# Optimization experiments

Hardware: AMD Instinct MI355X
Metric: run time of the kernel (lower is better)

## Reference

```python
import jax, jax.numpy as jnp
import numpy as np

ENC_HID = 512
DEC_HID = 1024
ATTN_DIM = 1024
ATTN_IN = ENC_HID * 2 + DEC_HID  # 2048
B, S = 32, 1024


def setup_inputs() -> dict:
    key = jax.random.key(0)
    k1, k2, k3, k4, k5 = jax.random.split(key, 5)
    decoder_hidden = jax.random.normal(k1, (B, DEC_HID), dtype=jnp.float32)
    encoder_outputs = jax.random.normal(k2, (B, S, 2 * ENC_HID), dtype=jnp.float32)
    # nn.Linear(attn_in, attn_dim): weight [attn_dim, attn_in], bias [attn_dim]
    lim = 1.0 / np.sqrt(ATTN_IN)
    W = jax.random.uniform(k3, (ATTN_IN, ATTN_DIM), jnp.float32, -lim, lim)
    b = jax.random.uniform(k4, (ATTN_DIM,), jnp.float32, -lim, lim)
    v = jax.random.uniform(k5, (ATTN_DIM,), jnp.float32, 0.0, 1.0)
    return {"decoder_hidden": decoder_hidden, "encoder_outputs": encoder_outputs,
            "W": W, "b": b, "v": v}


def reference(decoder_hidden, encoder_outputs, W, b, v):
    # Avoid materializing the repeat+concat: split the Linear weight into the
    # decoder-hidden block and the encoder-outputs block. Same math as
    # tanh(Linear(cat([dec_rep, enc], -1))).
    W_dec = W[:DEC_HID]          # [dec_hid, attn_dim]
    W_enc = W[DEC_HID:]          # [2*enc_hid, attn_dim]
    dec_proj = decoder_hidden @ W_dec + b                     # [B, A]
    enc_proj = jnp.einsum('bse,ea->bsa', encoder_outputs, W_enc)  # [B, S, A]
    energy = jnp.tanh(enc_proj + dec_proj[:, None, :])        # [B, S, A]
    attention = jnp.einsum('bsa,a->bs', energy, v)            # [B, S]
    return jax.nn.softmax(attention, axis=1)
```

## Files before the change

### kernel.cpp

```cpp
#include <hip/hip_runtime.h>
#include <stdint.h>

#define ENC2 1024
#define DECH 1024
#define ADIM 1024
#define BB   32
#define SS   1024

typedef _Float16 half_t;
typedef __attribute__((ext_vector_type(8))) _Float16 half8;
typedef __attribute__((ext_vector_type(4))) float    f32x4;

__device__ __forceinline__ void dma16(const half_t* g, half_t* l) {
    __builtin_amdgcn_global_load_lds((const __attribute__((address_space(1))) void*)g,
                                     (__attribute__((address_space(3))) void*)l,
                                     16, 0, 0);
}

__global__ __launch_bounds__(256) void k_wt(const float* __restrict__ W,
                                            half_t* __restrict__ Wt2) {
    __shared__ float tile[32][257];
    const int nb = blockIdx.x >> 5;
    const int ks = blockIdx.x & 31;
    const int t = threadIdx.x;
    #pragma unroll
    for (int i = 0; i < 32; i++) {
        int idx = t + i * 256;
        int kr = idx >> 8, n = idx & 255;
        tile[kr][n] = W[(size_t)(DECH + ks * 32 + kr) * ADIM + nb * 256 + n];
    }
    __syncthreads();
    half_t* reg = Wt2 + ((size_t)(nb * 32 + ks) << 13);
    #pragma unroll
    for (int i = 0; i < 4; i++) {
        int cid = t + i * 256;
        int r = cid >> 2, pos = cid & 3;
        int c = pos ^ ((r >> 1) & 3);
        half8 h;
        #pragma unroll
        for (int e = 0; e < 8; e++) h[e] = (half_t)tile[c * 8 + e][r];
        *(half8*)(reg + r * 32 + pos * 8) = h;
    }
}

__global__ __launch_bounds__(256) void k_dp1(const float* __restrict__ dh,
                                             const float* __restrict__ W,
                                             float* __restrict__ part) {
    __shared__ float red[4][BB][64];
    const int t = threadIdx.x;
    const int ct = blockIdx.x & 15;
    const int kc = blockIdx.x >> 4;
    const int col = ct * 64 + (t & 63);
    const int w = t >> 6;
    const int k0 = kc * 128 + w * 32;
    float wreg[32];
    #pragma unroll
    for (int kk = 0; kk < 32; kk++)
        wreg[kk] = W[(size_t)(k0 + kk) * ADIM + col];
    float s[BB];
    #pragma unroll
    for (int b = 0; b < BB; b++) s[b] = 0.f;
    #pragma unroll
    for (int kk = 0; kk < 32; kk++) {
        #pragma unroll
        for (int b = 0; b < BB; b++)
            s[b] += dh[b * DECH + k0 + kk] * wreg[kk];
    }
    #pragma unroll
    for (int b = 0; b < BB; b++) red[w][b][t & 63] = s[b];
    __syncthreads();
    if (t < 64) {
        for (int b = 0; b < BB; b++)
            part[((size_t)kc * BB + b) * ADIM + ct * 64 + t] =
                red[0][b][t] + red[1][b][t] + red[2][b][t] + red[3][b][t];
    }
}

__global__ __launch_bounds__(256) void k_dp2(const float* __restrict__ part,
                                             const float* __restrict__ bias,
                                             float* __restrict__ decp) {
    const int i = blockIdx.x * 256 + threadIdx.x;
    float s = bias[i & (ADIM - 1)];
    #pragma unroll
    for (int kc = 0; kc < 8; kc++)
        s += part[(size_t)kc * BB * ADIM + i];
    decp[i] = s;
}

#define BM 128
#define BN 256
#define BK 32
#define LDA 40

__global__ __launch_bounds__(512, 4) void k_main(const float* __restrict__ enc,
                                                 const half_t* __restrict__ Wt2,
                                                 const float* __restrict__ decp,
                                                 const float* __restrict__ v,
                                                 float* __restrict__ scores_part) {
    __shared__ half_t lsA[2][BM][LDA];
    __shared__ half_t lsB[2][BN * BK];

    const int bid = blockIdx.x;
    const int mi = (bid >> 5) * 8 + (bid & 7);
    const int nb = (bid >> 3) & 3;
    const int m0 = mi * BM;
    const int t = threadIdx.x;
    const int w = t >> 6, L = t & 63;
    const int wm = w & 1, wn = w >> 1;
    const int lane15 = L & 15, quad = L >> 4;

    const int arow = t & 127;
    const int akc  = (t >> 7) * 8;
    const float* Aptr = enc + (size_t)(m0 + arow) * ENC2 + akc;

    const half_t* Bbase = Wt2 + ((size_t)(nb * 32) << 13);

    f32x4 acc[4][4];
    #pragma unroll
    for (int i = 0; i < 4; i++)
        #pragma unroll
        for (int j = 0; j < 4; j++) acc[i][j] = (f32x4)0.f;

    float4 ra0, ra1;
    auto loadA = [&](int ks) {
        const float* p = Aptr + ks * BK;
        ra0 = *(const float4*)p;
        ra1 = *(const float4*)(p + 4);
    };
    auto writeA = [&](int pb) {
        half8 ha;
        ha[0] = (half_t)ra0.x; ha[1] = (half_t)ra0.y;
        ha[2] = (half_t)ra0.z; ha[3] = (half_t)ra0.w;
        ha[4] = (half_t)ra1.x; ha[5] = (half_t)ra1.y;
        ha[6] = (half_t)ra1.z; ha[7] = (half_t)ra1.w;
        *(half8*)&lsA[pb][arow][akc] = ha;
    };
    auto dmaB = [&](int ks, int pb) {
        #pragma unroll
        for (int jj = 0; jj < 2; jj++) {
            int j = 2 * w + jj;
            dma16(Bbase + ((size_t)ks << 13) + j * 512 + L * 8,
                  &lsB[pb][j * 512]);
        }
    };

    dmaB(0, 0);
    loadA(0);
    writeA(0);
    loadA(1);
    __syncthreads();

    for (int ks = 0; ks < ENC2 / BK; ks++) {
        const int cur = ks & 1;
        if (ks < ENC2 / BK - 1) {
            dmaB(ks + 1, cur ^ 1);
            writeA(cur ^ 1);
            if (ks < ENC2 / BK - 2) loadA(ks + 2);
        }
        half8 af[4], bf[4];
        #pragma unroll
        for (int sm = 0; sm < 4; sm++)
            af[sm] = *(const half8*)&lsA[cur][wm * 64 + sm * 16 + lane15][quad * 8];
        #pragma unroll
        for (int sn = 0; sn < 4; sn++) {
            int r = wn * 64 + sn * 16 + lane15;
            int pos = quad ^ ((r >> 1) & 3);
            bf[sn] = *(const half8*)&lsB[cur][r * 32 + pos * 8];
        }
        #pragma unroll
        for (int sm = 0; sm < 4; sm++)
            #pragma unroll
            for (int sn = 0; sn < 4; sn++)
                acc[sm][sn] = __builtin_amdgcn_mfma_f32_16x16x32_f16(
                    af[sm], bf[sn], acc[sm][sn], 0, 0, 0);
        __syncthreads();
    }

    const int batch = mi >> 3;
    float vv[4], dp[4];
    #pragma unroll
    for (int sn = 0; sn < 4; sn++) {
        int ng = nb * BN + wn * 64 + sn * 16 + lane15;
        vv[sn] = v[ng];
        dp[sn] = decp[(size_t)batch * ADIM + ng];
    }

    float* redL = (float*)&lsA[0][0][0];
    #pragma unroll
    for (int sm = 0; sm < 4; sm++) {
        #pragma unroll
        for (int rr = 0; rr < 4; rr++) {
            float s = 0.f;
            #pragma unroll
            for (int sn = 0; sn < 4; sn++) {
                float x = acc[sm][sn][rr] + dp[sn];
                float e  = __builtin_amdgcn_exp2f(x * 2.8853900817779268f);
                float th = 1.f - 2.f * __builtin_amdgcn_rcpf(e + 1.f);
                s += th * vv[sn];
            }
            s += __shfl_xor(s, 1, 64);
            s += __shfl_xor(s, 2, 64);
            s += __shfl_xor(s, 4, 64);
            s += __shfl_xor(s, 8, 64);
            if (lane15 == 0) {
                int mlocal = wm * 64 + sm * 16 + quad * 4 + rr;
                redL[wn * 128 + mlocal] = s;
            }
        }
    }
    __syncthreads();
    if (t < 128) {
        float s = redL[t] + redL[128 + t] + redL[256 + t] + redL[384 + t];
        scores_part[((size_t)nb << 15) + m0 + t] = s;
    }
}

__global__ __launch_bounds__(256) void k_softmax(const float* __restrict__ sp,
                                                 float* __restrict__ out) {
    __shared__ float red[8];
    const int b = blockIdx.x, t = threadIdx.x;
    float x[4];
    #pragma unroll
    for (int i = 0; i < 4; i++) {
        size_t idx = (size_t)b * SS + t + i * 256;
        x[i] = sp[idx] + sp[(1u << 15) + idx] + sp[(2u << 15) + idx] +
               sp[(3u << 15) + idx];
    }
    float mx = fmaxf(fmaxf(x[0], x[1]), fmaxf(x[2], x[3]));
    #pragma unroll
    for (int d = 1; d < 64; d <<= 1) mx = fmaxf(mx, __shfl_xor(mx, d, 64));
    if ((t & 63) == 0) red[t >> 6] = mx;
    __syncthreads();
    mx = fmaxf(fmaxf(red[0], red[1]), fmaxf(red[2], red[3]));
    float e[4], s = 0.f;
    #pragma unroll
    for (int i = 0; i < 4; i++) {
        e[i] = __builtin_amdgcn_exp2f((x[i] - mx) * 1.4426950408889634f);
        s += e[i];
    }
    #pragma unroll
    for (int d = 1; d < 64; d <<= 1) s += __shfl_xor(s, d, 64);
    if ((t & 63) == 0) red[4 + (t >> 6)] = s;
    __syncthreads();
    s = red[4] + red[5] + red[6] + red[7];
    float inv = 1.f / s;
    #pragma unroll
    for (int i = 0; i < 4; i++) out[(size_t)b * SS + t + i * 256] = e[i] * inv;
}

extern "C" void kernel_launch(void* const* d_in, const int* in_sizes, int n_in,
                              void* d_out, int out_size, void* d_ws, size_t ws_size,
                              hipStream_t stream) {
    const float* dh   = (const float*)d_in[0];
    const float* enc  = (const float*)d_in[1];
    const float* W    = (const float*)d_in[2];
    const float* bias = (const float*)d_in[3];
    const float* v    = (const float*)d_in[4];
    float* out = (float*)d_out;

    char* ws = (char*)d_ws;
    half_t* Wt2   = (half_t*)ws;
    float*  decp  = (float*)(ws + 2u * 1024 * 1024);
    float*  spart = (float*)(ws + 2u * 1024 * 1024 + 128 * 1024);
    float*  dpart = (float*)(ws + 2u * 1024 * 1024 + 640 * 1024);

    k_wt     <<<128, 256, 0, stream>>>(W, Wt2);
    k_dp1    <<<128, 256, 0, stream>>>(dh, W, dpart);
    k_dp2    <<<128, 256, 0, stream>>>(dpart, bias, decp);
    k_main   <<<1024, 512, 0, stream>>>(enc, Wt2, decp, v, spart);
    k_softmax<<<32, 256, 0, stream>>>(spart, out);
}
```

Baseline: 308.0 us.

## Merge prep kernels and fuse softmax into GEMM via last-block atomic counter

Folds the weight transpose and decoder-projection partials into one prep launch, and folds the dp2 bias reduction into the GEMM epilogue. The GEMM tile shrinks from 128x256 with 512 threads to 128x128 with 256 threads, doubling the grid, and each thread now loads 16 A floats. The separate softmax kernel is replaced by a per-batch atomic counter, so the last of the 64 blocks for a batch performs the softmax. This removes three launches and their gaps, but adds epilogue dpart reads, doubles the A-tile reloads across column blocks, and serialises the softmax tail on the last block per batch.

New measurement: 441.0 us. 1.43x slower.

```diff
diff --git a/kernel.cpp b/kernel.cpp
--- a/kernel.cpp
+++ b/kernel.cpp
@@ -17,103 +17,102 @@
                                      16, 0, 0);
 }
 
-__global__ __launch_bounds__(256) void k_wt(const float* __restrict__ W,
-                                            half_t* __restrict__ Wt2) {
-    __shared__ float tile[32][257];
-    const int nb = blockIdx.x >> 5;
-    const int ks = blockIdx.x & 31;
+__global__ __launch_bounds__(256) void k_prep(const float* __restrict__ W,
+                                              const float* __restrict__ dh,
+                                              half_t* __restrict__ Wt2,
+                                              float* __restrict__ dpart,
+                                              int* __restrict__ cnt) {
+    __shared__ __align__(16) char sm[32768];
+    const int bid = blockIdx.x;
     const int t = threadIdx.x;
-    #pragma unroll
-    for (int i = 0; i < 32; i++) {
-        int idx = t + i * 256;
-        int kr = idx >> 8, n = idx & 255;
-        tile[kr][n] = W[(size_t)(DECH + ks * 32 + kr) * ADIM + nb * 256 + n];
-    }
-    __syncthreads();
-    half_t* reg = Wt2 + ((size_t)(nb * 32 + ks) << 13);
-    #pragma unroll
-    for (int i = 0; i < 4; i++) {
-        int cid = t + i * 256;
-        int r = cid >> 2, pos = cid & 3;
-        int c = pos ^ ((r >> 1) & 3);
-        half8 h;
-        #pragma unroll
-        for (int e = 0; e < 8; e++) h[e] = (half_t)tile[c * 8 + e][r];
-        *(half8*)(reg + r * 32 + pos * 8) = h;
-    }
-}
-
-__global__ __launch_bounds__(256) void k_dp1(const float* __restrict__ dh,
-                                             const float* __restrict__ W,
-                                             float* __restrict__ part) {
-    __shared__ float red[4][BB][64];
-    const int t = threadIdx.x;
-    const int ct = blockIdx.x & 15;
-    const int kc = blockIdx.x >> 4;
-    const int col = ct * 64 + (t & 63);
-    const int w = t >> 6;
-    const int k0 = kc * 128 + w * 32;
-    float wreg[32];
-    #pragma unroll
-    for (int kk = 0; kk < 32; kk++)
-        wreg[kk] = W[(size_t)(k0 + kk) * ADIM + col];
-    float s[BB];
-    #pragma unroll
-    for (int b = 0; b < BB; b++) s[b] = 0.f;
-    #pragma unroll
-    for (int kk = 0; kk < 32; kk++) {
-        #pragma unroll
-        for (int b = 0; b < BB; b++)
-            s[b] += dh[b * DECH + k0 + kk] * wreg[kk];
-    }
-    #pragma unroll
-    for (int b = 0; b < BB; b++) red[w][b][t & 63] = s[b];
-    __syncthreads();
-    if (t < 64) {
-        for (int b = 0; b < BB; b++)
-            part[((size_t)kc * BB + b) * ADIM + ct * 64 + t] =
-                red[0][b][t] + red[1][b][t] + red[2][b][t] + red[3][b][t];
-    }
-}
-
-__global__ __launch_bounds__(256) void k_dp2(const float* __restrict__ part,
-                                             const float* __restrict__ bias,
-                                             float* __restrict__ decp) {
-    const int i = blockIdx.x * 256 + threadIdx.x;
-    float s = bias[i & (ADIM - 1)];
-    #pragma unroll
-    for (int kc = 0; kc < 8; kc++)
-        s += part[(size_t)kc * BB * ADIM + i];
-    decp[i] = s;
+    if (bid < 256) {
+        float (*tile)[129] = (float(*)[129])sm;
+        const int nb = bid >> 5, ks = bid & 31;
+        #pragma unroll
+        for (int i = 0; i < 16; i++) {
+            int idx = t + i * 256;
+            int kr = idx >> 7, n = idx & 127;
+            tile[kr][n] = W[(size_t)(DECH + ks * 32 + kr) * ADIM + nb * 128 + n];
+        }
+        __syncthreads();
+        half_t* reg = Wt2 + ((size_t)(nb * 32 + ks) << 12);
+        #pragma unroll
+        for (int i = 0; i < 2; i++) {
+            int cid = t + i * 256;
+            int r = cid >> 2, pos = cid & 3;
+            int c = pos ^ ((r >> 1) & 3);
+            half8 h;
+            #pragma unroll
+            for (int e = 0; e < 8; e++) h[e] = (half_t)tile[c * 8 + e][r];
+            *(half8*)(reg + r * 32 + pos * 8) = h;
+        }
+    } else if (bid < 384) {
+        float (*red)[BB][64] = (float(*)[BB][64])sm;
+        const int idx = bid - 256;
+        const int ct = idx & 15, kc = idx >> 4;
+        const int col = ct * 64 + (t & 63);
+        const int w = t >> 6;
+        const int k0 = kc * 128 + w * 32;
+        float wreg[32];
+        #pragma unroll
+        for (int kk = 0; kk < 32; kk++)
+            wreg[kk] = W[(size_t)(k0 + kk) * ADIM + col];
+        float s[BB];
+        #pragma unroll
+        for (int b = 0; b < BB; b++) s[b] = 0.f;
+        #pragma unroll
+        for (int kk = 0; kk < 32; kk++) {
+            #pragma unroll
+            for (int b = 0; b < BB; b++)
+                s[b] += dh[b * DECH + k0 + kk] * wreg[kk];
+        }
+        #pragma unroll
+        for (int b = 0; b < BB; b++) red[w][b][t & 63] = s[b];
+        __syncthreads();
+        if (t < 64) {
+            for (int b = 0; b < BB; b++)
+                dpart[((size_t)kc * BB + b) * ADIM + ct * 64 + t] =
+                    red[0][b][t] + red[1][b][t] + red[2][b][t] + red[3][b][t];
+        }
+    } else {
+        if (t < BB) cnt[t] = 0;
+    }
 }
 
 #define BM 128
-#define BN 256
+#define BN 128
 #define BK 32
 #define LDA 40
 
-__global__ __launch_bounds__(512, 4) void k_main(const float* __restrict__ enc,
+__global__ __launch_bounds__(256, 4) void k_main(const float* __restrict__ enc,
                                                  const half_t* __restrict__ Wt2,
-                                                 const float* __restrict__ decp,
+                                                 const float* __restrict__ dpart,
+                                                 const float* __restrict__ bias,
                                                  const float* __restrict__ v,
-                                                 float* __restrict__ scores_part) {
+                                                 float* __restrict__ spart,
+                                                 int* __restrict__ cnt,
+                                                 float* __restrict__ out) {
     __shared__ half_t lsA[2][BM][LDA];
     __shared__ half_t lsB[2][BN * BK];
+    __shared__ float sred[8];
+    __shared__ int sflag;
 
     const int bid = blockIdx.x;
-    const int mi = (bid >> 5) * 8 + (bid & 7);
-    const int nb = (bid >> 3) & 3;
+    const int mi = (bid >> 6) * 8 + (bid & 7);
+    const int nb = (bid >> 3) & 7;
     const int m0 = mi * BM;
+    const int n0 = nb * BN;
+    const int batch = mi >> 3;
     const int t = threadIdx.x;
     const int w = t >> 6, L = t & 63;
     const int wm = w & 1, wn = w >> 1;
     const int lane15 = L & 15, quad = L >> 4;
 
     const int arow = t & 127;
-    const int akc  = (t >> 7) * 8;
-    const float* Aptr = enc + (size_t)(m0 + arow) * ENC2 + akc;
-
-    const half_t* Bbase = Wt2 + ((size_t)(nb * 32) << 13);
+    const int ah   = (t >> 7) * 16;
+    const float* Aptr = enc + (size_t)(m0 + arow) * ENC2 + ah;
+
+    const half_t* Bbase = Wt2 + ((size_t)(nb * 32) << 12);
 
     f32x4 acc[4][4];
     #pragma unroll
@@ -121,32 +120,43 @@
         #pragma unroll
         for (int j = 0; j < 4; j++) acc[i][j] = (f32x4)0.f;
 
-    float4 ra0, ra1;
+    float4 ra[4];
+    half8 rh0, rh1;
     auto loadA = [&](int ks) {
         const float* p = Aptr + ks * BK;
-        ra0 = *(const float4*)p;
-        ra1 = *(const float4*)(p + 4);
+        ra[0] = ((const float4*)p)[0];
+        ra[1] = ((const float4*)p)[1];
+        ra[2] = ((const float4*)p)[2];
+        ra[3] = ((const float4*)p)[3];
+    };
+    auto cvtA = [&]() {
+        half8 h0, h1;
+        h0[0] = (half_t)ra[0].x; h0[1] = (half_t)ra[0].y;
+        h0[2] = (half_t)ra[0].z; h0[3] = (half_t)ra[0].w;
+        h0[4] = (half_t)ra[1].x; h0[5] = (half_t)ra[1].y;
+        h0[6] = (half_t)ra[1].z; h0[7] = (half_t)ra[1].w;
+        h1[0] = (half_t)ra[2].x; h1[1] = (half_t)ra[2].y;
+        h1[2] = (half_t)ra[2].z; h1[3] = (half_t)ra[2].w;
+        h1[4] = (half_t)ra[3].x; h1[5] = (half_t)ra[3].y;
+        h1[6] = (half_t)ra[3].z; h1[7] = (half_t)ra[3].w;
+        rh0 = h0; rh1 = h1;
     };
     auto writeA = [&](int pb) {
-        half8 ha;
-        ha[0] = (half_t)ra0.x; ha[1] = (half_t)ra0.y;
-        ha[2] = (half_t)ra0.z; ha[3] = (half_t)ra0.w;
-        ha[4] = (half_t)ra1.x; ha[5] = (half_t)ra1.y;
-        ha[6] = (half_t)ra1.z; ha[7] = (half_t)ra1.w;
-        *(half8*)&lsA[pb][arow][akc] = ha;
+        *(half8*)&lsA[pb][arow][ah]     = rh0;
+        *(half8*)&lsA[pb][arow][ah + 8] = rh1;
     };
     auto dmaB = [&](int ks, int pb) {
         #pragma unroll
         for (int jj = 0; jj < 2; jj++) {
             int j = 2 * w + jj;
-            dma16(Bbase + ((size_t)ks << 13) + j * 512 + L * 8,
+            dma16(Bbase + ((size_t)ks << 12) + j * 512 + L * 8,
                   &lsB[pb][j * 512]);
         }
     };
 
+    loadA(0);
     dmaB(0, 0);
-    loadA(0);
-    writeA(0);
+    cvtA(); writeA(0);
     loadA(1);
     __syncthreads();
 
@@ -154,13 +164,14 @@
         const int cur = ks & 1;
         if (ks < ENC2 / BK - 1) {
             dmaB(ks + 1, cur ^ 1);
+            cvtA();
             writeA(cur ^ 1);
             if (ks < ENC2 / BK - 2) loadA(ks + 2);
         }
         half8 af[4], bf[4];
         #pragma unroll
-        for (int sm = 0; sm < 4; sm++)
-            af[sm] = *(const half8*)&lsA[cur][wm * 64 + sm * 16 + lane15][quad * 8];
+        for (int sm2 = 0; sm2 < 4; sm2++)
+            af[sm2] = *(const half8*)&lsA[cur][wm * 64 + sm2 * 16 + lane15][quad * 8];
         #pragma unroll
         for (int sn = 0; sn < 4; sn++) {
             int r = wn * 64 + sn * 16 + lane15;
@@ -168,32 +179,35 @@
             bf[sn] = *(const half8*)&lsB[cur][r * 32 + pos * 8];
         }
         #pragma unroll
-        for (int sm = 0; sm < 4; sm++)
+        for (int sm2 = 0; sm2 < 4; sm2++)
             #pragma unroll
             for (int sn = 0; sn < 4; sn++)
-                acc[sm][sn] = __builtin_amdgcn_mfma_f32_16x16x32_f16(
-                    af[sm], bf[sn], acc[sm][sn], 0, 0, 0);
-        __syncthreads();
-    }
-
-    const int batch = mi >> 3;
+                acc[sm2][sn] = __builtin_amdgcn_mfma_f32_16x16x32_f16(
+                    af[sm2], bf[sn], acc[sm2][sn], 0, 0, 0);
+        __syncthreads();
+    }
+
     float vv[4], dp[4];
     #pragma unroll
     for (int sn = 0; sn < 4; sn++) {
-        int ng = nb * BN + wn * 64 + sn * 16 + lane15;
+        int ng = n0 + wn * 64 + sn * 16 + lane15;
         vv[sn] = v[ng];
-        dp[sn] = decp[(size_t)batch * ADIM + ng];
+        float d = bias[ng];
+        #pragma unroll
+        for (int kc = 0; kc < 8; kc++)
+            d += dpart[((size_t)kc * BB + batch) * ADIM + ng];
+        dp[sn] = d;
     }
 
     float* redL = (float*)&lsA[0][0][0];
     #pragma unroll
-    for (int sm = 0; sm < 4; sm++) {
+    for (int sm2 = 0; sm2 < 4; sm2++) {
         #pragma unroll
         for (int rr = 0; rr < 4; rr++) {
             float s = 0.f;
             #pragma unroll
             for (int sn = 0; sn < 4; sn++) {
-                float x = acc[sm][sn][rr] + dp[sn];
+                float x = acc[sm2][sn][rr] + dp[sn];
                 float e  = __builtin_amdgcn_exp2f(x * 2.8853900817779268f);
                 float th = 1.f - 2.f * __builtin_amdgcn_rcpf(e + 1.f);
                 s += th * vv[sn];
@@ -203,49 +217,55 @@
             s += __shfl_xor(s, 4, 64);
             s += __shfl_xor(s, 8, 64);
             if (lane15 == 0) {
-                int mlocal = wm * 64 + sm * 16 + quad * 4 + rr;
+                int mlocal = wm * 64 + sm2 * 16 + quad * 4 + rr;
                 redL[wn * 128 + mlocal] = s;
             }
         }
     }
     __syncthreads();
-    if (t < 128) {
-        float s = redL[t] + redL[128 + t] + redL[256 + t] + redL[384 + t];
-        scores_part[((size_t)nb << 15) + m0 + t] = s;
-    }
-}
-
-__global__ __launch_bounds__(256) void k_softmax(const float* __restrict__ sp,
-                                                 float* __restrict__ out) {
-    __shared__ float red[8];
-    const int b = blockIdx.x, t = threadIdx.x;
-    float x[4];
-    #pragma unroll
-    for (int i = 0; i < 4; i++) {
-        size_t idx = (size_t)b * SS + t + i * 256;
-        x[i] = sp[idx] + sp[(1u << 15) + idx] + sp[(2u << 15) + idx] +
-               sp[(3u << 15) + idx];
-    }
-    float mx = fmaxf(fmaxf(x[0], x[1]), fmaxf(x[2], x[3]));
-    #pragma unroll
-    for (int d = 1; d < 64; d <<= 1) mx = fmaxf(mx, __shfl_xor(mx, d, 64));
-    if ((t & 63) == 0) red[t >> 6] = mx;
-    __syncthreads();
-    mx = fmaxf(fmaxf(red[0], red[1]), fmaxf(red[2], red[3]));
-    float e[4], s = 0.f;
-    #pragma unroll
-    for (int i = 0; i < 4; i++) {
-        e[i] = __builtin_amdgcn_exp2f((x[i] - mx) * 1.4426950408889634f);
-        s += e[i];
-    }
-    #pragma unroll
-    for (int d = 1; d < 64; d <<= 1) s += __shfl_xor(s, d, 64);
-    if ((t & 63) == 0) red[4 + (t >> 6)] = s;
-    __syncthreads();
-    s = red[4] + red[5] + red[6] + red[7];
-    float inv = 1.f / s;
-    #pragma unroll
-    for (int i = 0; i < 4; i++) out[(size_t)b * SS + t + i * 256] = e[i] * inv;
+    if (t < 128)
+        spart[((size_t)nb << 15) + m0 + t] = redL[t] + redL[128 + t];
+    __syncthreads();
+
+    if (t == 0) {
+        __threadfence();
+        sflag = (atomicAdd(&cnt[batch], 1) == 63);
+    }
+    __syncthreads();
+    if (sflag) {
+        __threadfence();
+        float x[4];
+        #pragma unroll
+        for (int i = 0; i < 4; i++) {
+            size_t off = (size_t)batch * SS + t + i * 256;
+            float s = 0.f;
+            #pragma unroll
+            for (int n2 = 0; n2 < 8; n2++)
+                s += spart[((size_t)n2 << 15) + off];
+            x[i] = s;
+        }
+        float mx = fmaxf(fmaxf(x[0], x[1]), fmaxf(x[2], x[3]));
+        #pragma unroll
+        for (int d = 1; d < 64; d <<= 1) mx = fmaxf(mx, __shfl_xor(mx, d, 64));
+        if ((t & 63) == 0) sred[t >> 6] = mx;
+        __syncthreads();
+        mx = fmaxf(fmaxf(sred[0], sred[1]), fmaxf(sred[2], sred[3]));
+        float e[4], s = 0.f;
+        #pragma unroll
+        for (int i = 0; i < 4; i++) {
+            e[i] = __builtin_amdgcn_exp2f((x[i] - mx) * 1.4426950408889634f);
+            s += e[i];
+        }
+        #pragma unroll
+        for (int d = 1; d < 64; d <<= 1) s += __shfl_xor(s, d, 64);
+        if ((t & 63) == 0) sred[4 + (t >> 6)] = s;
+        __syncthreads();
+        s = sred[4] + sred[5] + sred[6] + sred[7];
+        float inv = 1.f / s;
+        #pragma unroll
+        for (int i = 0; i < 4; i++)
+            out[(size_t)batch * SS + t + i * 256] = e[i] * inv;
+    }
 }
 
 extern "C" void kernel_launch(void* const* d_in, const int* in_sizes, int n_in,
@@ -260,13 +280,10 @@
 
     char* ws = (char*)d_ws;
     half_t* Wt2   = (half_t*)ws;
-    float*  decp  = (float*)(ws + 2u * 1024 * 1024);
-    float*  spart = (float*)(ws + 2u * 1024 * 1024 + 128 * 1024);
-    float*  dpart = (float*)(ws + 2u * 1024 * 1024 + 640 * 1024);
-
-    k_wt     <<<128, 256, 0, stream>>>(W, Wt2);
-    k_dp1    <<<128, 256, 0, stream>>>(dh, W, dpart);
-    k_dp2    <<<128, 256, 0, stream>>>(dpart, bias, decp);
-    k_main   <<<1024, 512, 0, stream>>>(enc, Wt2, decp, v, spart);
-    k_softmax<<<32, 256, 0, stream>>>(spart, out);
-}
+    float*  dpart = (float*)(ws + (2u << 20));
+    float*  spart = (float*)(ws + (3u << 20));
+    int*    cnt   = (int*)(ws + (4u << 20));
+
+    k_prep<<<385,  256, 0, stream>>>(W, dh, Wt2, dpart, cnt);
+    k_main<<<2048, 256, 0, stream>>>(enc, Wt2, dpart, bias, v, spart, cnt, out);
+}
```
